# Performance work log

Measured on AMD Instinct MI355X. Metric: run time of the kernel, lower is better.

Reference implementation:

```python
import jax, jax.numpy as jnp
import numpy as np

EMB_DIM = 64
DICT_SIZE = 512
MOMENTUM = 0.99
EPS = 1e-05


def setup_inputs() -> dict:
    key = jax.random.key(0)
    k1, k2 = jax.random.split(key)
    inp = jax.random.normal(k1, (32, EMB_DIM, 64, 64), dtype=jnp.float32)
    embed = jax.random.normal(k2, (DICT_SIZE, EMB_DIM), dtype=jnp.float32)
    cluster_size = jnp.zeros((DICT_SIZE,), dtype=jnp.float32)
    embed_avg = embed.T  # torch: self.embed.T.clone()
    return {"input": inp, "embed": embed, "cluster_size": cluster_size, "embed_avg": embed_avg}


def reference(input, embed, cluster_size, embed_avg):
    b, c, h, w = input.shape
    D = embed.shape[0]
    # torch: input.transpose(1, -1).reshape(-1, emb_dim)  -> row order (b, w, h)
    flatten = jnp.swapaxes(input, 1, -1).reshape(-1, c)  # (N, c)
    # negative squared L2 scores (largest == nearest), as in _torch_knn
    scores = 2.0 * (flatten @ embed.T)                     # (N, D)
    scores = scores - jnp.sum(embed * embed, axis=1)[None, :]
    scores = scores - jnp.sum(flatten * flatten, axis=1)[:, None]
    ids_flat = jnp.argmax(scores, axis=1)                  # (N,) int
    # torch: ids.view(b, h, w) (quirk: flatten order is (b,w,h); h==w so shapes match)
    ids = ids_flat.reshape(b, h, w)
    # lookup: F.embedding(ids, embed).transpose(1, -1); the two transposes cancel
    quantized = jnp.swapaxes(embed[ids_flat].reshape(b, w, h, c), 1, -1)  # (b, c, h, w)
    commit_loss = jnp.mean(jnp.square(input - quantized))
    # EMA codebook statistics (training branch, done under no_grad in torch)
    onehot_sum = jax.ops.segment_sum(jnp.ones_like(ids_flat, dtype=flatten.dtype), ids_flat, num_segments=D)  # (D,)
    embed_sum = jax.ops.segment_sum(flatten, ids_flat, num_segments=D).T  # (c, D) == flatten.T @ onehot
    new_cluster_size = cluster_size * MOMENTUM + onehot_sum * (1.0 - MOMENTUM)
    new_embed_avg = embed_avg * MOMENTUM + embed_sum * (1.0 - MOMENTUM)
    n = jnp.sum(new_cluster_size)
    cs = n * (new_cluster_size + EPS) / (n + D * EPS)
    new_embed = new_embed_avg.T / cs[:, None]
    return quantized, commit_loss, ids, new_embed, new_cluster_size, new_embed_avg
```

## Files before the change

### kernel.cpp

```cpp
#include <hip/hip_runtime.h>

#define EMB 64
#define DICT 512
#define HW 4096
#define NPTS (32 * HW)
#define MOM 0.99f
#define OMOM 0.01f
#define EPSV 1e-5f

typedef float v4f __attribute__((ext_vector_type(4)));
typedef unsigned int uint;
typedef uint uint4v __attribute__((ext_vector_type(4)));
typedef short short8 __attribute__((ext_vector_type(8)));
typedef __bf16 bf16x8 __attribute__((ext_vector_type(8)));
typedef float f32x4 __attribute__((ext_vector_type(4)));

#define WS_COMMIT 0
#define WS_COUNTS 64
#define WS_ESUM   1024
#define WS_ZERO_FLOATS 33792
#define WS_EE     33792
#define WS_EHG    34320
#define WS_IDS    67600

#define PS 520
#define TB 4160
#define PSX 260

#define ESCALE 65536.0f
#define EINV   (1.0f / 65536.0f)

__device__ __forceinline__ uint bf16rne(float x) {
    uint u = __float_as_uint(x);
    return (u + 0x7fffu + ((u >> 16) & 1u)) >> 16;
}

__device__ __forceinline__ bf16x8 ldfragg(const uint* s, int idx) {
    return __builtin_bit_cast(bf16x8, *(const short8*)(s + idx));
}

__global__ __launch_bounds__(256) void vq_prep(const float* __restrict__ embed,
                                               float* __restrict__ ws,
                                               uint* __restrict__ ehg,
                                               float* __restrict__ ee) {
    int t = threadIdx.x;
    int blk = blockIdx.x;
    for (int i = blk * 256 + t; i < WS_ZERO_FLOATS; i += 32 * 256) ws[i] = 0.f;

    int jl = t >> 4;
    int ci = t & 15;
    int j  = blk * 16 + jl;
    float nrm = 0.f;
    #pragma unroll
    for (int it = 0; it < 2; ++it) {
        int c2 = ci + it * 16;
        float x0 = embed[j * 64 + 2 * c2];
        float x1 = embed[j * 64 + 2 * c2 + 1];
        nrm = fmaf(x0, x0, nrm);
        nrm = fmaf(x1, x1, nrm);
        uint h0 = bf16rne(x0), h1 = bf16rne(x1);
        int plane = (c2 >> 4) * 4 + ((c2 >> 2) & 3);
        int idx = (j >> 7) * TB + plane * PS + (j & 127) * 4 + (c2 & 3);
        ehg[idx] = h0 | (h1 << 16);
    }
    #pragma unroll
    for (int off = 8; off > 0; off >>= 1) nrm += __shfl_xor(nrm, off, 16);
    if (ci == 0) ee[j] = nrm;
}

__global__ __launch_bounds__(256, 8) void vq_argmax(
    const float* __restrict__ input, const uint* __restrict__ ehg,
    const float* __restrict__ ee, const float* __restrict__ embed,
    float* __restrict__ out_q, float* __restrict__ out_ids,
    int* __restrict__ ws_ids, float* __restrict__ ws) {
    __shared__ float sX[16 * PSX];
    __shared__ float sEE[512];
    __shared__ int sCand[128];
    __shared__ float sRes[128];
    __shared__ float cred[4];

    int t = threadIdx.x;
    int blk = blockIdx.x;
    int b = blk >> 6, h = blk & 63;

    const float* xg = input + (size_t)b * (EMB * HW) + h * 64;

    {
        int p = t & 63;
        int pg = t >> 6;
        #pragma unroll
        for (int i = 0; i < 4; ++i) {
            int plane = pg * 4 + i;
            v4f v;
            #pragma unroll
            for (int c = 0; c < 4; ++c)
                v[c] = xg[(size_t)(plane * 4 + c) * HW + p];
            *(v4f*)&sX[plane * PSX + p * 4] = v;
        }
        sEE[t] = ee[t];
        sEE[t + 256] = ee[t + 256];
    }
    __syncthreads();

    int l = t & 63, wv = t >> 6;
    int g = l >> 4, col = l & 15;
    int row = wv * 16 + col;

    bf16x8 Ah[2];
    #pragma unroll
    for (int kh = 0; kh < 2; ++kh) {
        int p0 = kh * 8 + g * 2;
        v4f xa = *(const v4f*)&sX[p0 * PSX + row * 4];
        v4f xb = *(const v4f*)&sX[(p0 + 1) * PSX + row * 4];
        uint4v fr;
        fr[0] = bf16rne(xa[0]) | (bf16rne(xa[1]) << 16);
        fr[1] = bf16rne(xa[2]) | (bf16rne(xa[3]) << 16);
        fr[2] = bf16rne(xb[0]) | (bf16rne(xb[1]) << 16);
        fr[3] = bf16rne(xb[2]) | (bf16rne(xb[3]) << 16);
        Ah[kh] = __builtin_bit_cast(bf16x8, fr);
    }

    float tb1[4], tb2[4];
    #pragma unroll
    for (int r = 0; r < 4; ++r) { tb1[r] = -3.0e38f; tb2[r] = -3.0e38f; }

    for (int jt = 0; jt < 4; ++jt) {
        const uint* eh = ehg + jt * TB;
        #pragma unroll
        for (int nt = 0; nt < 8; ++nt) {
            bf16x8 Bh0 = ldfragg(eh, (0 * 4 + g) * PS + (nt * 16 + col) * 4);
            bf16x8 Bh1 = ldfragg(eh, (1 * 4 + g) * PS + (nt * 16 + col) * 4);
            float e2 = -0.5f * sEE[jt * 128 + nt * 16 + col];
            f32x4 acc = {e2, e2, e2, e2};
            acc = __builtin_amdgcn_mfma_f32_16x16x32_bf16(Ah[0], Bh0, acc, 0, 0, 0);
            acc = __builtin_amdgcn_mfma_f32_16x16x32_bf16(Ah[1], Bh1, acc, 0, 0, 0);
            uint tag = (uint)(511 - (jt * 128 + nt * 16 + col));
            #pragma unroll
            for (int r = 0; r < 4; ++r) {
                float sp = __uint_as_float(
                    (__float_as_uint(acc[r]) & 0xFFFFFE00u) | tag);
                float o1 = tb1[r];
                tb1[r] = fmaxf(sp, o1);
                tb2[r] = __builtin_amdgcn_fmed3f(sp, o1, tb2[r]);
            }
        }
    }

    #pragma unroll
    for (int r = 0; r < 4; ++r) {
        float t1 = tb1[r], t2 = tb2[r];
        #pragma unroll
        for (int off = 8; off > 0; off >>= 1) {
            float o1 = __shfl_xor(t1, off, 16);
            float o2 = __shfl_xor(t2, off, 16);
            float hi = fmaxf(t1, o1);
            float lo = fminf(t1, o1);
            t2 = fmaxf(lo, fmaxf(t2, o2));
            t1 = hi;
        }
        if (col == 0) {
            int p = wv * 16 + g * 4 + r;
            sCand[p * 2]     = 511 - (int)(__float_as_uint(t1) & 511u);
            sCand[p * 2 + 1] = 511 - (int)(__float_as_uint(t2) & 511u);
        }
    }
    __syncthreads();

    int p = t & 63, wc = (t >> 6) & 1;
    int c = 0;
    if (t < 128) {
        c = sCand[p * 2 + wc];
        const v4f* erow = (const v4f*)(embed + c * 64);
        float dot = 0.f;
        #pragma unroll
        for (int plane = 0; plane < 16; ++plane) {
            v4f xq = *(const v4f*)&sX[plane * PSX + p * 4];
            v4f e4 = erow[plane];
            dot = fmaf(xq[0], e4[0], dot);
            dot = fmaf(xq[1], e4[1], dot);
            dot = fmaf(xq[2], e4[2], dot);
            dot = fmaf(xq[3], e4[3], dot);
        }
        sRes[t] = fmaf(2.f, dot, -sEE[c]);
    }
    __syncthreads();

    float cl = 0.f;
    if (t < 128) {
        float sx = sRes[t];
        float so = sRes[t ^ 64];
        int co = sCand[p * 2 + (1 - wc)];
        bool win = (sx > so) || (sx == so && c < co);
        if (win) {
            ws_ids[b * HW + h * 64 + p] = c;
            out_ids[b * HW + p * 64 + h] = (float)c;
            float* qg = out_q + (size_t)b * (EMB * HW) + h * 64 + p;
            const v4f* erow = (const v4f*)(embed + c * 64);
            #pragma unroll
            for (int plane = 0; plane < 16; ++plane) {
                v4f xq = *(const v4f*)&sX[plane * PSX + p * 4];
                v4f e4 = erow[plane];
                #pragma unroll
                for (int v = 0; v < 4; ++v) {
                    int ch = plane * 4 + v;
                    qg[(size_t)ch * HW] = e4[v];
                    float d = xq[v] - e4[v];
                    cl = fmaf(d, d, cl);
                }
            }
        }
    }
    #pragma unroll
    for (int off = 32; off > 0; off >>= 1) cl += __shfl_down(cl, off);
    if ((t & 63) == 0) cred[t >> 6] = cl;
    __syncthreads();
    if (t == 0)
        unsafeAtomicAdd(&ws[WS_COMMIT], (cred[0] + cred[1]) + (cred[2] + cred[3]));
}

__global__ __launch_bounds__(256) void vq_stats(
    const float* __restrict__ input, const int* __restrict__ ws_ids,
    float* __restrict__ ws) {
    __shared__ uint es[2 * 520];
    __shared__ uint cnt_s[DICT];

    int t = threadIdx.x;
    int bc = blockIdx.x;
    int b = bc >> 5, cg = bc & 31;

    #pragma unroll
    for (int i = t; i < 2 * 520; i += 256) es[i] = 0u;
    if (cg == 0)
        for (int i = t; i < DICT; i += 256) cnt_s[i] = 0u;

    const int* idg = ws_ids + b * HW;
    int4 idv[4];
    #pragma unroll
    for (int it = 0; it < 4; ++it)
        idv[it] = *(const int4*)(idg + (t + it * 256) * 4);
    __syncthreads();

    #pragma unroll
    for (int chl = 0; chl < 2; ++chl) {
        const float* xg = input + (size_t)b * (EMB * HW) + (size_t)(cg * 2 + chl) * HW;
        uint* esr = es + chl * 520;
        #pragma unroll
        for (int it = 0; it < 4; ++it) {
            v4f x = *(const v4f*)(xg + (t + it * 256) * 4);
            atomicAdd(&esr[idv[it].x], (uint)__float2int_rn(x.x * ESCALE));
            atomicAdd(&esr[idv[it].y], (uint)__float2int_rn(x.y * ESCALE));
            atomicAdd(&esr[idv[it].z], (uint)__float2int_rn(x.z * ESCALE));
            atomicAdd(&esr[idv[it].w], (uint)__float2int_rn(x.w * ESCALE));
        }
    }
    if (cg == 0) {
        #pragma unroll
        for (int it = 0; it < 4; ++it) {
            atomicAdd(&cnt_s[idv[it].x], 1u);
            atomicAdd(&cnt_s[idv[it].y], 1u);
            atomicAdd(&cnt_s[idv[it].z], 1u);
            atomicAdd(&cnt_s[idv[it].w], 1u);
        }
    }
    __syncthreads();

    #pragma unroll
    for (int i = t; i < 2 * DICT; i += 256) {
        int chl = i >> 9, j = i & 511;
        int v = (int)es[chl * 520 + j];
        if (v != 0)
            unsafeAtomicAdd(&ws[WS_ESUM + (cg * 2 + chl) * DICT + j],
                            (float)v * EINV);
    }
    if (cg == 0)
        for (int i = t; i < DICT; i += 256) {
            uint c = cnt_s[i];
            if (c != 0u) unsafeAtomicAdd(&ws[WS_COUNTS + i], (float)c);
        }
}

__global__ __launch_bounds__(256) void vq_fin(
    const float* __restrict__ embed_avg, const float* __restrict__ cluster_size,
    const float* __restrict__ ws, float* __restrict__ out_embed,
    float* __restrict__ out_cs, float* __restrict__ out_avg,
    float* __restrict__ out_loss) {
    __shared__ float red[256];
    int t = threadIdx.x, blk = blockIdx.x;

    float ncs0 = cluster_size[t] * MOM + ws[WS_COUNTS + t] * OMOM;
    float ncs1 = cluster_size[t + 256] * MOM + ws[WS_COUNTS + t + 256] * OMOM;
    if (blk == 0) {
        out_cs[t] = ncs0;
        out_cs[t + 256] = ncs1;
        if (t == 0)
            out_loss[0] = ws[WS_COMMIT] * (1.0f / (float)((size_t)NPTS * EMB));
    }
    red[t] = ncs0 + ncs1;
    __syncthreads();
    #pragma unroll
    for (int off = 128; off > 0; off >>= 1) {
        if (t < off) red[t] += red[t + off];
        __syncthreads();
    }
    float n = red[0];

    int idx = blk * 256 + t;
    int ch = idx >> 9, d = idx & 511;
    float avg = embed_avg[idx] * MOM + ws[WS_ESUM + idx] * OMOM;
    out_avg[idx] = avg;
    float ncs = cluster_size[d] * MOM + ws[WS_COUNTS + d] * OMOM;
    float cs = n * (ncs + EPSV) / (n + (float)DICT * EPSV);
    out_embed[d * EMB + ch] = avg / cs;
}

extern "C" void kernel_launch(void* const* d_in, const int* in_sizes, int n_in,
                              void* d_out, int out_size, void* d_ws, size_t ws_size,
                              hipStream_t stream) {
    const float* input        = (const float*)d_in[0];
    const float* embed        = (const float*)d_in[1];
    const float* cluster_size = (const float*)d_in[2];
    const float* embed_avg    = (const float*)d_in[3];

    float* out   = (float*)d_out;
    float* q     = out;
    float* loss  = out + 8388608;
    float* ids   = out + 8388609;
    float* oemb  = out + 8519681;
    float* ocs   = out + 8552449;
    float* oavg  = out + 8552961;
    float* ws    = (float*)d_ws;

    vq_prep  <<<32, 256, 0, stream>>>(embed, ws, (uint*)(ws + WS_EHG), ws + WS_EE);
    vq_argmax<<<2048, 256, 0, stream>>>(input, (const uint*)(ws + WS_EHG),
                                        ws + WS_EE, embed, q, ids,
                                        (int*)(ws + WS_IDS), ws);
    vq_stats <<<1024, 256, 0, stream>>>(input, (const int*)(ws + WS_IDS), ws);
    vq_fin   <<<128, 256, 0, stream>>>(embed_avg, cluster_size, ws, oemb, ocs,
                                       oavg, loss);
}
```

Measured before the change: 79.15 us.

## Split codebook across waves instead of points, merge top-2 candidates via LDS

```diff
diff --git a/kernel.cpp b/kernel.cpp
--- a/kernel.cpp
+++ b/kernel.cpp
@@ -68,13 +68,14 @@
     if (ci == 0) ee[j] = nrm;
 }
 
-__global__ __launch_bounds__(256, 8) void vq_argmax(
+__global__ __launch_bounds__(256, 4) void vq_argmax(
     const float* __restrict__ input, const uint* __restrict__ ehg,
     const float* __restrict__ ee, const float* __restrict__ embed,
     float* __restrict__ out_q, float* __restrict__ out_ids,
     int* __restrict__ ws_ids, float* __restrict__ ws) {
     __shared__ float sX[16 * PSX];
     __shared__ float sEE[512];
+    __shared__ float sMrg[4][64][2];
     __shared__ int sCand[128];
     __shared__ float sRes[128];
     __shared__ float cred[4];
@@ -104,65 +105,88 @@
 
     int l = t & 63, wv = t >> 6;
     int g = l >> 4, col = l & 15;
-    int row = wv * 16 + col;
-
-    bf16x8 Ah[2];
-    #pragma unroll
-    for (int kh = 0; kh < 2; ++kh) {
-        int p0 = kh * 8 + g * 2;
-        v4f xa = *(const v4f*)&sX[p0 * PSX + row * 4];
-        v4f xb = *(const v4f*)&sX[(p0 + 1) * PSX + row * 4];
-        uint4v fr;
-        fr[0] = bf16rne(xa[0]) | (bf16rne(xa[1]) << 16);
-        fr[1] = bf16rne(xa[2]) | (bf16rne(xa[3]) << 16);
-        fr[2] = bf16rne(xb[0]) | (bf16rne(xb[1]) << 16);
-        fr[3] = bf16rne(xb[2]) | (bf16rne(xb[3]) << 16);
-        Ah[kh] = __builtin_bit_cast(bf16x8, fr);
-    }
-
-    float tb1[4], tb2[4];
-    #pragma unroll
-    for (int r = 0; r < 4; ++r) { tb1[r] = -3.0e38f; tb2[r] = -3.0e38f; }
-
-    for (int jt = 0; jt < 4; ++jt) {
-        const uint* eh = ehg + jt * TB;
-        #pragma unroll
-        for (int nt = 0; nt < 8; ++nt) {
-            bf16x8 Bh0 = ldfragg(eh, (0 * 4 + g) * PS + (nt * 16 + col) * 4);
-            bf16x8 Bh1 = ldfragg(eh, (1 * 4 + g) * PS + (nt * 16 + col) * 4);
-            float e2 = -0.5f * sEE[jt * 128 + nt * 16 + col];
+
+    bf16x8 Ah[4][2];
+    #pragma unroll
+    for (int mt = 0; mt < 4; ++mt)
+        #pragma unroll
+        for (int kh = 0; kh < 2; ++kh) {
+            int row = mt * 16 + col;
+            int p0 = kh * 8 + g * 2;
+            v4f xa = *(const v4f*)&sX[p0 * PSX + row * 4];
+            v4f xb = *(const v4f*)&sX[(p0 + 1) * PSX + row * 4];
+            uint4v fr;
+            fr[0] = bf16rne(xa[0]) | (bf16rne(xa[1]) << 16);
+            fr[1] = bf16rne(xa[2]) | (bf16rne(xa[3]) << 16);
+            fr[2] = bf16rne(xb[0]) | (bf16rne(xb[1]) << 16);
+            fr[3] = bf16rne(xb[2]) | (bf16rne(xb[3]) << 16);
+            Ah[mt][kh] = __builtin_bit_cast(bf16x8, fr);
+        }
+
+    float tb1[4][4], tb2[4][4];
+    #pragma unroll
+    for (int mt = 0; mt < 4; ++mt)
+        #pragma unroll
+        for (int r = 0; r < 4; ++r) { tb1[mt][r] = -3.0e38f; tb2[mt][r] = -3.0e38f; }
+
+    const uint* eh = ehg + wv * TB;
+    #pragma unroll
+    for (int nt = 0; nt < 8; ++nt) {
+        bf16x8 Bh0 = ldfragg(eh, (0 * 4 + g) * PS + (nt * 16 + col) * 4);
+        bf16x8 Bh1 = ldfragg(eh, (1 * 4 + g) * PS + (nt * 16 + col) * 4);
+        float e2 = -0.5f * sEE[wv * 128 + nt * 16 + col];
+        uint tag = (uint)(511 - (wv * 128 + nt * 16 + col));
+        #pragma unroll
+        for (int mt = 0; mt < 4; ++mt) {
             f32x4 acc = {e2, e2, e2, e2};
-            acc = __builtin_amdgcn_mfma_f32_16x16x32_bf16(Ah[0], Bh0, acc, 0, 0, 0);
-            acc = __builtin_amdgcn_mfma_f32_16x16x32_bf16(Ah[1], Bh1, acc, 0, 0, 0);
-            uint tag = (uint)(511 - (jt * 128 + nt * 16 + col));
+            acc = __builtin_amdgcn_mfma_f32_16x16x32_bf16(Ah[mt][0], Bh0, acc, 0, 0, 0);
+            acc = __builtin_amdgcn_mfma_f32_16x16x32_bf16(Ah[mt][1], Bh1, acc, 0, 0, 0);
             #pragma unroll
             for (int r = 0; r < 4; ++r) {
                 float sp = __uint_as_float(
                     (__float_as_uint(acc[r]) & 0xFFFFFE00u) | tag);
-                float o1 = tb1[r];
-                tb1[r] = fmaxf(sp, o1);
-                tb2[r] = __builtin_amdgcn_fmed3f(sp, o1, tb2[r]);
+                float o1 = tb1[mt][r];
+                tb1[mt][r] = fmaxf(sp, o1);
+                tb2[mt][r] = __builtin_amdgcn_fmed3f(sp, o1, tb2[mt][r]);
             }
         }
     }
 
     #pragma unroll
-    for (int r = 0; r < 4; ++r) {
-        float t1 = tb1[r], t2 = tb2[r];
-        #pragma unroll
-        for (int off = 8; off > 0; off >>= 1) {
-            float o1 = __shfl_xor(t1, off, 16);
-            float o2 = __shfl_xor(t2, off, 16);
-            float hi = fmaxf(t1, o1);
-            float lo = fminf(t1, o1);
-            t2 = fmaxf(lo, fmaxf(t2, o2));
-            t1 = hi;
-        }
-        if (col == 0) {
-            int p = wv * 16 + g * 4 + r;
-            sCand[p * 2]     = 511 - (int)(__float_as_uint(t1) & 511u);
-            sCand[p * 2 + 1] = 511 - (int)(__float_as_uint(t2) & 511u);
-        }
+    for (int mt = 0; mt < 4; ++mt)
+        #pragma unroll
+        for (int r = 0; r < 4; ++r) {
+            float t1 = tb1[mt][r], t2 = tb2[mt][r];
+            #pragma unroll
+            for (int off = 8; off > 0; off >>= 1) {
+                float o1 = __shfl_xor(t1, off, 16);
+                float o2 = __shfl_xor(t2, off, 16);
+                float hi = fmaxf(t1, o1);
+                float lo = fminf(t1, o1);
+                t2 = fmaxf(lo, fmaxf(t2, o2));
+                t1 = hi;
+            }
+            if (col == 0) {
+                int p = mt * 16 + g * 4 + r;
+                sMrg[wv][p][0] = t1;
+                sMrg[wv][p][1] = t2;
+            }
+        }
+    __syncthreads();
+
+    if (t < 64) {
+        float a1 = sMrg[0][t][0], a2 = sMrg[0][t][1];
+        float b1 = sMrg[1][t][0], b2 = sMrg[1][t][1];
+        float c1 = sMrg[2][t][0], c2 = sMrg[2][t][1];
+        float d1 = sMrg[3][t][0], d2 = sMrg[3][t][1];
+        float m1 = fmaxf(a1, b1);
+        float m2 = fmaxf(fminf(a1, b1), fmaxf(a2, b2));
+        float n1 = fmaxf(c1, d1);
+        float n2 = fmaxf(fminf(c1, d1), fmaxf(c2, d2));
+        float t1 = fmaxf(m1, n1);
+        float t2 = fmaxf(fminf(m1, n1), fmaxf(m2, n2));
+        sCand[t * 2]     = 511 - (int)(__float_as_uint(t1) & 511u);
+        sCand[t * 2 + 1] = 511 - (int)(__float_as_uint(t2) & 511u);
     }
     __syncthreads();
 
```

Measured after the change: 86.92 us. 1.1x slower.

## Split codebook across wave pairs with 2 row tiles per wave for B-fragment reuse

Applied to the files above, without the earlier changes.

```diff
diff --git a/kernel.cpp b/kernel.cpp
--- a/kernel.cpp
+++ b/kernel.cpp
@@ -68,13 +68,14 @@
     if (ci == 0) ee[j] = nrm;
 }
 
-__global__ __launch_bounds__(256, 8) void vq_argmax(
+__global__ __launch_bounds__(256, 7) void vq_argmax(
     const float* __restrict__ input, const uint* __restrict__ ehg,
     const float* __restrict__ ee, const float* __restrict__ embed,
     float* __restrict__ out_q, float* __restrict__ out_ids,
     int* __restrict__ ws_ids, float* __restrict__ ws) {
     __shared__ float sX[16 * PSX];
     __shared__ float sEE[512];
+    __shared__ float sMrg[2][64][2];
     __shared__ int sCand[128];
     __shared__ float sRes[128];
     __shared__ float cred[4];
@@ -104,65 +105,88 @@
 
     int l = t & 63, wv = t >> 6;
     int g = l >> 4, col = l & 15;
-    int row = wv * 16 + col;
-
-    bf16x8 Ah[2];
-    #pragma unroll
-    for (int kh = 0; kh < 2; ++kh) {
-        int p0 = kh * 8 + g * 2;
-        v4f xa = *(const v4f*)&sX[p0 * PSX + row * 4];
-        v4f xb = *(const v4f*)&sX[(p0 + 1) * PSX + row * 4];
-        uint4v fr;
-        fr[0] = bf16rne(xa[0]) | (bf16rne(xa[1]) << 16);
-        fr[1] = bf16rne(xa[2]) | (bf16rne(xa[3]) << 16);
-        fr[2] = bf16rne(xb[0]) | (bf16rne(xb[1]) << 16);
-        fr[3] = bf16rne(xb[2]) | (bf16rne(xb[3]) << 16);
-        Ah[kh] = __builtin_bit_cast(bf16x8, fr);
-    }
-
-    float tb1[4], tb2[4];
-    #pragma unroll
-    for (int r = 0; r < 4; ++r) { tb1[r] = -3.0e38f; tb2[r] = -3.0e38f; }
-
-    for (int jt = 0; jt < 4; ++jt) {
+    int mh = wv >> 1;
+    int jh = wv & 1;
+
+    bf16x8 Ah[2][2];
+    #pragma unroll
+    for (int mtl = 0; mtl < 2; ++mtl)
+        #pragma unroll
+        for (int kh = 0; kh < 2; ++kh) {
+            int row = mh * 32 + mtl * 16 + col;
+            int p0 = kh * 8 + g * 2;
+            v4f xa = *(const v4f*)&sX[p0 * PSX + row * 4];
+            v4f xb = *(const v4f*)&sX[(p0 + 1) * PSX + row * 4];
+            uint4v fr;
+            fr[0] = bf16rne(xa[0]) | (bf16rne(xa[1]) << 16);
+            fr[1] = bf16rne(xa[2]) | (bf16rne(xa[3]) << 16);
+            fr[2] = bf16rne(xb[0]) | (bf16rne(xb[1]) << 16);
+            fr[3] = bf16rne(xb[2]) | (bf16rne(xb[3]) << 16);
+            Ah[mtl][kh] = __builtin_bit_cast(bf16x8, fr);
+        }
+
+    float tb1[2][4], tb2[2][4];
+    #pragma unroll
+    for (int mtl = 0; mtl < 2; ++mtl)
+        #pragma unroll
+        for (int r = 0; r < 4; ++r) { tb1[mtl][r] = -3.0e38f; tb2[mtl][r] = -3.0e38f; }
+
+    #pragma unroll
+    for (int jtl = 0; jtl < 2; ++jtl) {
+        int jt = jh * 2 + jtl;
         const uint* eh = ehg + jt * TB;
         #pragma unroll
         for (int nt = 0; nt < 8; ++nt) {
             bf16x8 Bh0 = ldfragg(eh, (0 * 4 + g) * PS + (nt * 16 + col) * 4);
             bf16x8 Bh1 = ldfragg(eh, (1 * 4 + g) * PS + (nt * 16 + col) * 4);
             float e2 = -0.5f * sEE[jt * 128 + nt * 16 + col];
-            f32x4 acc = {e2, e2, e2, e2};
-            acc = __builtin_amdgcn_mfma_f32_16x16x32_bf16(Ah[0], Bh0, acc, 0, 0, 0);
-            acc = __builtin_amdgcn_mfma_f32_16x16x32_bf16(Ah[1], Bh1, acc, 0, 0, 0);
             uint tag = (uint)(511 - (jt * 128 + nt * 16 + col));
             #pragma unroll
-            for (int r = 0; r < 4; ++r) {
-                float sp = __uint_as_float(
-                    (__float_as_uint(acc[r]) & 0xFFFFFE00u) | tag);
-                float o1 = tb1[r];
-                tb1[r] = fmaxf(sp, o1);
-                tb2[r] = __builtin_amdgcn_fmed3f(sp, o1, tb2[r]);
+            for (int mtl = 0; mtl < 2; ++mtl) {
+                f32x4 acc = {e2, e2, e2, e2};
+                acc = __builtin_amdgcn_mfma_f32_16x16x32_bf16(Ah[mtl][0], Bh0, acc, 0, 0, 0);
+                acc = __builtin_amdgcn_mfma_f32_16x16x32_bf16(Ah[mtl][1], Bh1, acc, 0, 0, 0);
+                #pragma unroll
+                for (int r = 0; r < 4; ++r) {
+                    float sp = __uint_as_float(
+                        (__float_as_uint(acc[r]) & 0xFFFFFE00u) | tag);
+                    float o1 = tb1[mtl][r];
+                    tb1[mtl][r] = fmaxf(sp, o1);
+                    tb2[mtl][r] = __builtin_amdgcn_fmed3f(sp, o1, tb2[mtl][r]);
+                }
             }
         }
     }
 
     #pragma unroll
-    for (int r = 0; r < 4; ++r) {
-        float t1 = tb1[r], t2 = tb2[r];
-        #pragma unroll
-        for (int off = 8; off > 0; off >>= 1) {
-            float o1 = __shfl_xor(t1, off, 16);
-            float o2 = __shfl_xor(t2, off, 16);
-            float hi = fmaxf(t1, o1);
-            float lo = fminf(t1, o1);
-            t2 = fmaxf(lo, fmaxf(t2, o2));
-            t1 = hi;
-        }
-        if (col == 0) {
-            int p = wv * 16 + g * 4 + r;
-            sCand[p * 2]     = 511 - (int)(__float_as_uint(t1) & 511u);
-            sCand[p * 2 + 1] = 511 - (int)(__float_as_uint(t2) & 511u);
-        }
+    for (int mtl = 0; mtl < 2; ++mtl)
+        #pragma unroll
+        for (int r = 0; r < 4; ++r) {
+            float t1 = tb1[mtl][r], t2 = tb2[mtl][r];
+            #pragma unroll
+            for (int off = 8; off > 0; off >>= 1) {
+                float o1 = __shfl_xor(t1, off, 16);
+                float o2 = __shfl_xor(t2, off, 16);
+                float hi = fmaxf(t1, o1);
+                float lo = fminf(t1, o1);
+                t2 = fmaxf(lo, fmaxf(t2, o2));
+                t1 = hi;
+            }
+            if (col == 0) {
+                int p = mh * 32 + mtl * 16 + g * 4 + r;
+                sMrg[jh][p][0] = t1;
+                sMrg[jh][p][1] = t2;
+            }
+        }
+    __syncthreads();
+
+    if (t < 64) {
+        float a1 = sMrg[0][t][0], a2 = sMrg[0][t][1];
+        float b1 = sMrg[1][t][0], b2 = sMrg[1][t][1];
+        float t1 = fmaxf(a1, b1);
+        float t2 = fmaxf(fminf(a1, b1), fmaxf(a2, b2));
+        sCand[t * 2]     = 511 - (int)(__float_as_uint(t1) & 511u);
+        sCand[t * 2 + 1] = 511 - (int)(__float_as_uint(t2) & 511u);
     }
     __syncthreads();
 
```

Measured after the change: 259.1 us. 227% more time.
